# Performance work log

Hardware: AMD Instinct MI355X
Metric: run time of the kernel (lower is better)

## Reference

```python
import jax, jax.numpy as jnp
import numpy as np

N, C, S = 262144, 256, 16
BN_EPS = 1e-5


def setup_inputs() -> dict:
    key = jax.random.key(0)
    ks = jax.random.split(key, 8)
    x = jax.random.normal(ks[0], (N, C), dtype=jnp.float32)
    # strictly increasing cumulative offsets ending at N (guarantees nonzero counts)
    rng = np.random.default_rng(0)
    cuts = np.sort(rng.choice(np.arange(1, N), size=S - 1, replace=False))
    o = jnp.asarray(np.concatenate([cuts, [N]]), dtype=jnp.int64)
    # linear2_: Linear(C, C) (+ReLU, no BN in this branch)
    W2 = jax.random.normal(ks[1], (C, C), dtype=jnp.float32) / np.sqrt(C)
    b2 = jax.random.normal(ks[2], (C,), dtype=jnp.float32) * 0.01
    # linear1_: Linear(2C, C) + BatchNorm1d(C) + ReLU
    W1 = jax.random.normal(ks[3], (2 * C, C), dtype=jnp.float32) / np.sqrt(2 * C)
    b1 = jax.random.normal(ks[4], (C,), dtype=jnp.float32) * 0.01
    gamma = jnp.ones((C,), dtype=jnp.float32)
    beta = jnp.zeros((C,), dtype=jnp.float32)
    run_mean = jax.random.normal(ks[5], (C,), dtype=jnp.float32) * 0.01
    run_var = jnp.ones((C,), dtype=jnp.float32)
    return {"x": x, "o": o, "W2": W2, "b2": b2, "W1": W1, "b1": b1,
            "gamma": gamma, "beta": beta, "run_mean": run_mean, "run_var": run_var}


def reference(x, o, W2, b2, W1, b1, gamma, beta, run_mean, run_var):
    n, c = x.shape
    num_seg = o.shape[0]
    # segment id of each point: first offset strictly greater than index
    seg_ids = jnp.searchsorted(o, jnp.arange(n), side="right")  # [N]
    counts = jnp.diff(o, prepend=0).astype(x.dtype)             # [S]
    sums = jax.ops.segment_sum(x, seg_ids, num_segments=num_seg)  # [S, C]
    means = sums / counts[:, None]
    # linear2_ on per-segment mean, broadcast back to points
    h = jax.nn.relu(means @ W2 + b2)                            # [S, C]
    xc = jnp.concatenate([x, h[seg_ids]], axis=1)               # [N, 2C]
    # linear1_: Linear + BatchNorm1d (inference, running stats) + ReLU
    y = xc @ W1 + b1
    y = (y - run_mean) * jax.lax.rsqrt(run_var + BN_EPS) * gamma + beta
    return jax.nn.relu(y)
```

## Files before the change

### kernel.cpp

```cpp
#include <hip/hip_runtime.h>

#define C_DIM 256
#define S_SEG 16

typedef __attribute__((ext_vector_type(8))) short bf16x8;
typedef __attribute__((ext_vector_type(4))) float f32x4;

__device__ __forceinline__ short f2bf(float f) {
    unsigned u = __builtin_bit_cast(unsigned, f);
    u += 0x7FFF + ((u >> 16) & 1);
    return (short)(u >> 16);
}

__device__ __forceinline__ int o_get(const int* __restrict__ o_raw, int i) {
    return (o_raw[1] == 0) ? o_raw[2 * i] : o_raw[i];
}

__global__ __launch_bounds__(256) void k1_segsum(const float* __restrict__ x,
                                                 const int* __restrict__ o_raw,
                                                 float* __restrict__ sums) {
    __shared__ int o_s[S_SEG];
    __shared__ float4 partv[256];
    __shared__ int pseg[256];
    int t = threadIdx.x;
    if (t < S_SEG) o_s[t] = o_get(o_raw, t);
    __syncthreads();

    int rsub = t >> 6, cg = t & 63;
    int row0 = blockIdx.x * 256 + rsub * 64;
    const float4* xv = (const float4*)x;

    int cur = 0;
#pragma unroll
    for (int j = 0; j < S_SEG; ++j) cur += (row0 >= o_s[j]);
    int next = o_s[cur];

    float4 acc = make_float4(0.f, 0.f, 0.f, 0.f);
    for (int i = 0; i < 64; ++i) {
        int row = row0 + i;
        if (row >= next) {
            atomicAdd(&sums[cur * C_DIM + cg * 4 + 0], acc.x);
            atomicAdd(&sums[cur * C_DIM + cg * 4 + 1], acc.y);
            atomicAdd(&sums[cur * C_DIM + cg * 4 + 2], acc.z);
            atomicAdd(&sums[cur * C_DIM + cg * 4 + 3], acc.w);
            acc = make_float4(0.f, 0.f, 0.f, 0.f);
            do { cur++; next = o_s[cur]; } while (row >= next);
        }
        float4 v = xv[row * 64 + cg];
        acc.x += v.x; acc.y += v.y; acc.z += v.z; acc.w += v.w;
    }
    partv[t] = acc;
    pseg[t] = cur;
    __syncthreads();

    if (t < 64) {
        float4 a = partv[t];
        int s = pseg[t];
        for (int i = 1; i < 4; ++i) {
            int idx = i * 64 + t;
            int s2 = pseg[idx];
            float4 a2 = partv[idx];
            if (s2 == s) {
                a.x += a2.x; a.y += a2.y; a.z += a2.z; a.w += a2.w;
            } else {
                atomicAdd(&sums[s * C_DIM + t * 4 + 0], a.x);
                atomicAdd(&sums[s * C_DIM + t * 4 + 1], a.y);
                atomicAdd(&sums[s * C_DIM + t * 4 + 2], a.z);
                atomicAdd(&sums[s * C_DIM + t * 4 + 3], a.w);
                s = s2; a = a2;
            }
        }
        atomicAdd(&sums[s * C_DIM + t * 4 + 0], a.x);
        atomicAdd(&sums[s * C_DIM + t * 4 + 1], a.y);
        atomicAdd(&sums[s * C_DIM + t * 4 + 2], a.z);
        atomicAdd(&sums[s * C_DIM + t * 4 + 3], a.w);
    }
}

__global__ __launch_bounds__(256) void k2_small(const float* __restrict__ sums,
                                                const int* __restrict__ o_raw,
                                                const float* __restrict__ W2,
                                                const float* __restrict__ b2,
                                                const float* __restrict__ W1,
                                                const float* __restrict__ b1,
                                                const float* __restrict__ gamma,
                                                const float* __restrict__ beta,
                                                const float* __restrict__ rmean,
                                                const float* __restrict__ rvar,
                                                float* __restrict__ Cseg,
                                                short* __restrict__ W1s) {
    int t = threadIdx.x;
    int blk = blockIdx.x;
    if (blk < S_SEG) {
        __shared__ float mean_s[C_DIM];
        __shared__ float h_s[C_DIM];
        int s = blk;
        int lo = (s == 0) ? 0 : o_get(o_raw, s - 1);
        float inv = 1.0f / (float)(o_get(o_raw, s) - lo);
        mean_s[t] = sums[s * C_DIM + t] * inv;
        __syncthreads();
        float acc = b2[t];
#pragma unroll 4
        for (int k = 0; k < C_DIM; ++k) acc = fmaf(mean_s[k], W2[k * C_DIM + t], acc);
        h_s[t] = fmaxf(acc, 0.0f);
        __syncthreads();
        float acc2 = 0.f;
#pragma unroll 4
        for (int k = 0; k < C_DIM; ++k) acc2 = fmaf(h_s[k], W1[(C_DIM + k) * C_DIM + t], acc2);
        float sc = gamma[t] * rsqrtf(rvar[t] + 1e-5f);
        Cseg[s * C_DIM + t] = (b1[t] + acc2 - rmean[t]) * sc + beta[t];
    } else {
        int base = (blk - S_SEG) * 8192;
        for (int i = 0; i < 32; ++i) {
            int idx = base + i * 256 + t;
            int k = idx >> 8, c = idx & 255;
            float sc = gamma[c] * rsqrtf(rvar[c] + 1e-5f);
            float v = W1[k * C_DIM + c] * sc;
            int kb2 = k >> 5, q = (k >> 3) & 3, j = k & 7, nsub = c >> 4, r = c & 15;
            int off = ((kb2 * 16 + nsub) * 64 + q * 16 + r) * 8 + j;
            W1s[off] = f2bf(v);
        }
    }
}

__global__ __launch_bounds__(256) void k3_gemm(const float* __restrict__ x,
                                               const short* __restrict__ W1s,
                                               const float* __restrict__ Cseg,
                                               const int* __restrict__ o_raw,
                                               float* __restrict__ out) {
    __shared__ __align__(16) short As[2][4 * 2 * 64 * 8];
    __shared__ int o_s[S_SEG];

    int t = threadIdx.x;
    int wave = t >> 6, lane = t & 63;
    int q = lane >> 4, r = lane & 15;
    int wc = wave;
    int m0 = (int)(gridDim.x - 1 - blockIdx.x) * 64;

    if (t < S_SEG) o_s[t] = o_get(o_raw, t);

    f32x4 acc[4][4];
#pragma unroll
    for (int mt = 0; mt < 4; ++mt)
#pragma unroll
        for (int nt = 0; nt < 4; ++nt)
            acc[mt][nt] = (f32x4){0.f, 0.f, 0.f, 0.f};

    const float4* xv = (const float4*)x;
    int arow = t >> 3;
    int akc = t & 7;
    int kt_w = akc >> 2, q_w = akc & 3;
    int mt0 = arow >> 4, r0 = arow & 15;
    int slot0 = (mt0 * 2 + kt_w) * 64 + q_w * 16 + (r0 ^ q_w);
    int row1 = 32 + arow, mt1 = row1 >> 4, r1 = row1 & 15;
    int slot1 = (mt1 * 2 + kt_w) * 64 + q_w * 16 + (r1 ^ q_w);
    long gbase0 = (long)(m0 + arow) * 64 + akc * 2;
    long gbase1 = (long)(m0 + 32 + arow) * 64 + akc * 2;

    float4 c00, c01, c10, c11;
    c00 = xv[gbase0]; c01 = xv[gbase0 + 1];
    c10 = xv[gbase1]; c11 = xv[gbase1 + 1];
    {
        bf16x8 w0, w1;
        w0[0] = f2bf(c00.x); w0[1] = f2bf(c00.y); w0[2] = f2bf(c00.z); w0[3] = f2bf(c00.w);
        w0[4] = f2bf(c01.x); w0[5] = f2bf(c01.y); w0[6] = f2bf(c01.z); w0[7] = f2bf(c01.w);
        *(bf16x8*)&As[0][slot0 * 8] = w0;
        w1[0] = f2bf(c10.x); w1[1] = f2bf(c10.y); w1[2] = f2bf(c10.z); w1[3] = f2bf(c10.w);
        w1[4] = f2bf(c11.x); w1[5] = f2bf(c11.y); w1[6] = f2bf(c11.z); w1[7] = f2bf(c11.w);
        *(bf16x8*)&As[0][slot1 * 8] = w1;
    }
    __syncthreads();

    for (int kb = 0; kb < 4; ++kb) {
        if (kb < 3) {
            long o = (long)(kb + 1) * 16;
            c00 = xv[gbase0 + o]; c01 = xv[gbase0 + o + 1];
            c10 = xv[gbase1 + o]; c11 = xv[gbase1 + o + 1];
        }
        const short* Ab = As[kb & 1];
#pragma unroll
        for (int kt = 0; kt < 2; ++kt) {
            bf16x8 a[4], b[4];
#pragma unroll
            for (int mt = 0; mt < 4; ++mt)
                a[mt] = *(const bf16x8*)&Ab[((mt * 2 + kt) * 64 + q * 16 + (r ^ q)) * 8];
#pragma unroll
            for (int nt = 0; nt < 4; ++nt)
                b[nt] = *(const bf16x8*)&W1s[(((kb * 2 + kt) * 16 + wc * 4 + nt) * 64 + lane) * 8];
#pragma unroll
            for (int mt = 0; mt < 4; ++mt)
#pragma unroll
                for (int nt = 0; nt < 4; ++nt)
                    acc[mt][nt] = __builtin_amdgcn_mfma_f32_16x16x32_bf16(a[mt], b[nt], acc[mt][nt], 0, 0, 0);
        }
        if (kb < 3) {
            short* Aw = As[(kb + 1) & 1];
            bf16x8 w0, w1;
            w0[0] = f2bf(c00.x); w0[1] = f2bf(c00.y); w0[2] = f2bf(c00.z); w0[3] = f2bf(c00.w);
            w0[4] = f2bf(c01.x); w0[5] = f2bf(c01.y); w0[6] = f2bf(c01.z); w0[7] = f2bf(c01.w);
            *(bf16x8*)&Aw[slot0 * 8] = w0;
            w1[0] = f2bf(c10.x); w1[1] = f2bf(c10.y); w1[2] = f2bf(c10.z); w1[3] = f2bf(c10.w);
            w1[4] = f2bf(c11.x); w1[5] = f2bf(c11.y); w1[6] = f2bf(c11.z); w1[7] = f2bf(c11.w);
            *(bf16x8*)&Aw[slot1 * 8] = w1;
            __syncthreads();
        }
    }

#pragma unroll
    for (int mt = 0; mt < 4; ++mt) {
#pragma unroll
        for (int i = 0; i < 4; ++i) {
            int row = m0 + mt * 16 + q * 4 + i;
            int s = 0;
#pragma unroll
            for (int j = 0; j < S_SEG; ++j) s += (row >= o_s[j]);
#pragma unroll
            for (int nt = 0; nt < 4; ++nt) {
                int col = wc * 64 + nt * 16 + r;
                float v = acc[mt][nt][i] + Cseg[s * C_DIM + col];
                __builtin_nontemporal_store(fmaxf(v, 0.0f), &out[(long)row * C_DIM + col]);
            }
        }
    }
}

extern "C" void kernel_launch(void* const* d_in, const int* in_sizes, int n_in,
                              void* d_out, int out_size, void* d_ws, size_t ws_size,
                              hipStream_t stream) {
    const float* x     = (const float*)d_in[0];
    const int*   o     = (const int*)d_in[1];
    const float* W2    = (const float*)d_in[2];
    const float* b2    = (const float*)d_in[3];
    const float* W1    = (const float*)d_in[4];
    const float* b1    = (const float*)d_in[5];
    const float* gamma = (const float*)d_in[6];
    const float* beta  = (const float*)d_in[7];
    const float* rmean = (const float*)d_in[8];
    const float* rvar  = (const float*)d_in[9];
    float* out = (float*)d_out;

    float* sums = (float*)d_ws;
    float* Cseg = (float*)((char*)d_ws + 16384);
    short* W1s  = (short*)((char*)d_ws + 65536);

    hipMemsetAsync(d_ws, 0, 16384, stream);
    k1_segsum<<<1024, 256, 0, stream>>>(x, o, sums);
    k2_small<<<24, 256, 0, stream>>>(sums, o, W2, b2, W1, b1, gamma, beta, rmean, rvar, Cseg, W1s);
    k3_gemm<<<4096, 256, 0, stream>>>(x, W1s, Cseg, o, out);
}
```

Baseline: 600.9 us.

## Fuse bf16 conversion of x into segsum pass and drop GEMM LDS staging

The segment-sum kernel now also converts each x element to bf16 and writes it to workspace, already laid out in the MFMA fragment order. The GEMM kernel then reads A fragments straight from global memory instead of converting fp32 to bf16 and staging through double-buffered LDS with barriers. This removes the per-tile conversion work and synchronisation from the GEMM. In exchange it adds a 128MB bf16 intermediate written and re-read through global memory, and all four waves in a block load the same A fragments without sharing them. It also assumes the workspace is large enough for that buffer.

```diff
diff --git a/kernel.cpp b/kernel.cpp
--- a/kernel.cpp
+++ b/kernel.cpp
@@ -16,9 +16,10 @@
     return (o_raw[1] == 0) ? o_raw[2 * i] : o_raw[i];
 }
 
-__global__ __launch_bounds__(256) void k1_segsum(const float* __restrict__ x,
-                                                 const int* __restrict__ o_raw,
-                                                 float* __restrict__ sums) {
+__global__ __launch_bounds__(256) void k1_segsum_conv(const float* __restrict__ x,
+                                                      const int* __restrict__ o_raw,
+                                                      float* __restrict__ sums,
+                                                      short* __restrict__ xb) {
     __shared__ int o_s[S_SEG];
     __shared__ float4 partv[256];
     __shared__ int pseg[256];
@@ -27,6 +28,7 @@
     __syncthreads();
 
     int rsub = t >> 6, cg = t & 63;
+    int ktg = cg >> 3, q = (cg >> 1) & 3, j0 = (cg & 1) * 4;
     int row0 = blockIdx.x * 256 + rsub * 64;
     const float4* xv = (const float4*)x;
 
@@ -48,6 +50,12 @@
         }
         float4 v = xv[row * 64 + cg];
         acc.x += v.x; acc.y += v.y; acc.z += v.z; acc.w += v.w;
+        unsigned lo = (unsigned)(unsigned short)f2bf(v.x) |
+                      ((unsigned)(unsigned short)f2bf(v.y) << 16);
+        unsigned hi = (unsigned)(unsigned short)f2bf(v.z) |
+                      ((unsigned)(unsigned short)f2bf(v.w) << 16);
+        long off = ((long)((row >> 4) * 8 + ktg) * 64 + q * 16 + (row & 15)) * 8 + j0;
+        *(uint2*)&xb[off] = make_uint2(lo, hi);
     }
     partv[t] = acc;
     pseg[t] = cur;
@@ -116,28 +124,27 @@
             int k = idx >> 8, c = idx & 255;
             float sc = gamma[c] * rsqrtf(rvar[c] + 1e-5f);
             float v = W1[k * C_DIM + c] * sc;
-            int kb2 = k >> 5, q = (k >> 3) & 3, j = k & 7, nsub = c >> 4, r = c & 15;
-            int off = ((kb2 * 16 + nsub) * 64 + q * 16 + r) * 8 + j;
+            int ktg = k >> 5, q = (k >> 3) & 3, j = k & 7, nsub = c >> 4, r = c & 15;
+            int off = ((ktg * 16 + nsub) * 64 + q * 16 + r) * 8 + j;
             W1s[off] = f2bf(v);
         }
     }
 }
 
-__global__ __launch_bounds__(256) void k3_gemm(const float* __restrict__ x,
+__global__ __launch_bounds__(256) void k3_gemm(const short* __restrict__ xb,
                                                const short* __restrict__ W1s,
                                                const float* __restrict__ Cseg,
                                                const int* __restrict__ o_raw,
                                                float* __restrict__ out) {
-    __shared__ __align__(16) short As[2][4 * 2 * 64 * 8];
     __shared__ int o_s[S_SEG];
-
     int t = threadIdx.x;
     int wave = t >> 6, lane = t & 63;
     int q = lane >> 4, r = lane & 15;
-    int wc = wave;
     int m0 = (int)(gridDim.x - 1 - blockIdx.x) * 64;
+    int tile0 = m0 >> 4;
 
     if (t < S_SEG) o_s[t] = o_get(o_raw, t);
+    __syncthreads();
 
     f32x4 acc[4][4];
 #pragma unroll
@@ -146,64 +153,23 @@
         for (int nt = 0; nt < 4; ++nt)
             acc[mt][nt] = (f32x4){0.f, 0.f, 0.f, 0.f};
 
-    const float4* xv = (const float4*)x;
-    int arow = t >> 3;
-    int akc = t & 7;
-    int kt_w = akc >> 2, q_w = akc & 3;
-    int mt0 = arow >> 4, r0 = arow & 15;
-    int slot0 = (mt0 * 2 + kt_w) * 64 + q_w * 16 + (r0 ^ q_w);
-    int row1 = 32 + arow, mt1 = row1 >> 4, r1 = row1 & 15;
-    int slot1 = (mt1 * 2 + kt_w) * 64 + q_w * 16 + (r1 ^ q_w);
-    long gbase0 = (long)(m0 + arow) * 64 + akc * 2;
-    long gbase1 = (long)(m0 + 32 + arow) * 64 + akc * 2;
-
-    float4 c00, c01, c10, c11;
-    c00 = xv[gbase0]; c01 = xv[gbase0 + 1];
-    c10 = xv[gbase1]; c11 = xv[gbase1 + 1];
-    {
-        bf16x8 w0, w1;
-        w0[0] = f2bf(c00.x); w0[1] = f2bf(c00.y); w0[2] = f2bf(c00.z); w0[3] = f2bf(c00.w);
-        w0[4] = f2bf(c01.x); w0[5] = f2bf(c01.y); w0[6] = f2bf(c01.z); w0[7] = f2bf(c01.w);
-        *(bf16x8*)&As[0][slot0 * 8] = w0;
-        w1[0] = f2bf(c10.x); w1[1] = f2bf(c10.y); w1[2] = f2bf(c10.z); w1[3] = f2bf(c10.w);
-        w1[4] = f2bf(c11.x); w1[5] = f2bf(c11.y); w1[6] = f2bf(c11.z); w1[7] = f2bf(c11.w);
-        *(bf16x8*)&As[0][slot1 * 8] = w1;
-    }
-    __syncthreads();
-
-    for (int kb = 0; kb < 4; ++kb) {
-        if (kb < 3) {
-            long o = (long)(kb + 1) * 16;
-            c00 = xv[gbase0 + o]; c01 = xv[gbase0 + o + 1];
-            c10 = xv[gbase1 + o]; c11 = xv[gbase1 + o + 1];
-        }
-        const short* Ab = As[kb & 1];
-#pragma unroll
-        for (int kt = 0; kt < 2; ++kt) {
-            bf16x8 a[4], b[4];
-#pragma unroll
-            for (int mt = 0; mt < 4; ++mt)
-                a[mt] = *(const bf16x8*)&Ab[((mt * 2 + kt) * 64 + q * 16 + (r ^ q)) * 8];
+    const bf16x8* A = (const bf16x8*)xb;
+    const bf16x8* B = (const bf16x8*)W1s;
+
+#pragma unroll
+    for (int ktg = 0; ktg < 8; ++ktg) {
+        bf16x8 a[4], b[4];
+#pragma unroll
+        for (int mt = 0; mt < 4; ++mt)
+            a[mt] = A[((long)(tile0 + mt) * 8 + ktg) * 64 + lane];
+#pragma unroll
+        for (int nt = 0; nt < 4; ++nt)
+            b[nt] = B[(ktg * 16 + wave * 4 + nt) * 64 + lane];
+#pragma unroll
+        for (int mt = 0; mt < 4; ++mt)
 #pragma unroll
             for (int nt = 0; nt < 4; ++nt)
-                b[nt] = *(const bf16x8*)&W1s[(((kb * 2 + kt) * 16 + wc * 4 + nt) * 64 + lane) * 8];
-#pragma unroll
-            for (int mt = 0; mt < 4; ++mt)
-#pragma unroll
-                for (int nt = 0; nt < 4; ++nt)
-                    acc[mt][nt] = __builtin_amdgcn_mfma_f32_16x16x32_bf16(a[mt], b[nt], acc[mt][nt], 0, 0, 0);
-        }
-        if (kb < 3) {
-            short* Aw = As[(kb + 1) & 1];
-            bf16x8 w0, w1;
-            w0[0] = f2bf(c00.x); w0[1] = f2bf(c00.y); w0[2] = f2bf(c00.z); w0[3] = f2bf(c00.w);
-            w0[4] = f2bf(c01.x); w0[5] = f2bf(c01.y); w0[6] = f2bf(c01.z); w0[7] = f2bf(c01.w);
-            *(bf16x8*)&Aw[slot0 * 8] = w0;
-            w1[0] = f2bf(c10.x); w1[1] = f2bf(c10.y); w1[2] = f2bf(c10.z); w1[3] = f2bf(c10.w);
-            w1[4] = f2bf(c11.x); w1[5] = f2bf(c11.y); w1[6] = f2bf(c11.z); w1[7] = f2bf(c11.w);
-            *(bf16x8*)&Aw[slot1 * 8] = w1;
-            __syncthreads();
-        }
+                acc[mt][nt] = __builtin_amdgcn_mfma_f32_16x16x32_bf16(a[mt], b[nt], acc[mt][nt], 0, 0, 0);
     }
 
 #pragma unroll
@@ -216,7 +182,7 @@
             for (int j = 0; j < S_SEG; ++j) s += (row >= o_s[j]);
 #pragma unroll
             for (int nt = 0; nt < 4; ++nt) {
-                int col = wc * 64 + nt * 16 + r;
+                int col = wave * 64 + nt * 16 + r;
                 float v = acc[mt][nt][i] + Cseg[s * C_DIM + col];
                 __builtin_nontemporal_store(fmaxf(v, 0.0f), &out[(long)row * C_DIM + col]);
             }
@@ -242,9 +208,10 @@
     float* sums = (float*)d_ws;
     float* Cseg = (float*)((char*)d_ws + 16384);
     short* W1s  = (short*)((char*)d_ws + 65536);
+    short* xb   = (short*)((char*)d_ws + (2u << 20));
 
     hipMemsetAsync(d_ws, 0, 16384, stream);
-    k1_segsum<<<1024, 256, 0, stream>>>(x, o, sums);
+    k1_segsum_conv<<<1024, 256, 0, stream>>>(x, o, sums, xb);
     k2_small<<<24, 256, 0, stream>>>(sums, o, W2, b2, W1, b1, gamma, beta, rmean, rvar, Cseg, W1s);
-    k3_gemm<<<4096, 256, 0, stream>>>(x, W1s, Cseg, o, out);
-}
+    k3_gemm<<<4096, 256, 0, stream>>>(xb, W1s, Cseg, o, out);
+}
```

Result: slower. 720.4 us (+19.9%).
